# Kernel optimization log

Hardware: AMD Instinct MI355X
Metric: run time of the kernel (lower is better)

Reference implementation:

```python
import jax, jax.numpy as jnp
import numpy as np

B, T, C, H, W, NC = 128, 32, 512, 8, 32, 6625
HH = C // 2  # per-direction LSTM hidden


def setup_inputs() -> dict:
    key = jax.random.key(0)
    ks = jax.random.split(key, 20)
    u = lambda k, shape, n: jax.random.uniform(k, shape, jnp.float32, -1.0 / np.sqrt(n), 1.0 / np.sqrt(n))
    return dict(
        feature=jax.random.normal(ks[0], (B, C, H, W), jnp.float32),
        attention_map=jax.random.uniform(ks[1], (B, T, H, W), jnp.float32) + 1e-3,
        text=jax.random.randint(ks[2], (B, T), 0, NC),
        text_length=jnp.full((B,), T, dtype=jnp.int32),
        char_embeddings=jax.random.normal(ks[3], (NC, C), jnp.float32),
        lstm_w_ih_f=u(ks[4], (4 * HH, C), HH),
        lstm_w_hh_f=u(ks[5], (4 * HH, HH), HH),
        lstm_b_ih_f=u(ks[6], (4 * HH,), HH),
        lstm_b_hh_f=u(ks[7], (4 * HH,), HH),
        lstm_w_ih_b=u(ks[8], (4 * HH, C), HH),
        lstm_w_hh_b=u(ks[9], (4 * HH, HH), HH),
        lstm_b_ih_b=u(ks[10], (4 * HH,), HH),
        lstm_b_hh_b=u(ks[11], (4 * HH,), HH),
        gru_w_ih=u(ks[12], (3 * C, 2 * C), C),
        gru_w_hh=u(ks[13], (3 * C, C), C),
        gru_b_ih=u(ks[14], (3 * C,), C),
        gru_b_hh=u(ks[15], (3 * C,), C),
        gen_w=u(ks[16], (NC, C), C),
        gen_b=u(ks[17], (NC,), C),
    )


def _lstm_dir(xs, w_ih, w_hh, b_ih, b_hh):
    # xs: [T, B, C] -> hs: [T, B, HH]; PyTorch gate order i, f, g, o
    b = xs.shape[1]
    hh = w_hh.shape[1]
    def step(carry, xt):
        h, c = carry
        g = xt @ w_ih.T + h @ w_hh.T + (b_ih + b_hh)
        i, f, gg, o = jnp.split(g, 4, axis=-1)
        c = jax.nn.sigmoid(f) * c + jax.nn.sigmoid(i) * jnp.tanh(gg)
        h = jax.nn.sigmoid(o) * jnp.tanh(c)
        return (h, c), h
    h0 = jnp.zeros((b, hh), xs.dtype)
    _, hs = jax.lax.scan(step, (h0, h0), xs)
    return hs


def reference(feature, attention_map, text, text_length, char_embeddings,
              lstm_w_ih_f, lstm_w_hh_f, lstm_b_ih_f, lstm_b_hh_f,
              lstm_w_ih_b, lstm_w_hh_b, lstm_b_ih_b, lstm_b_hh_b,
              gru_w_ih, gru_w_hh, gru_b_ih, gru_b_hh, gen_w, gen_b):
    b, c, h, w = feature.shape
    t = attention_map.shape[1]
    # normalize attention over spatial dims, attention-pool features: [T, B, C]
    att = attention_map / attention_map.sum(axis=(2, 3), keepdims=True)
    cseq = jnp.einsum('bchw,bthw->tbc', feature, att)
    # bidirectional LSTM (dropout is identity in eval mode)
    hs_f = _lstm_dir(cseq, lstm_w_ih_f, lstm_w_hh_f, lstm_b_ih_f, lstm_b_hh_f)
    hs_b = _lstm_dir(cseq[::-1], lstm_w_ih_b, lstm_w_hh_b, lstm_b_ih_b, lstm_b_hh_b)[::-1]
    cseq = jnp.concatenate([hs_f, hs_b], axis=-1)  # [T, B, C]
    # teacher-forced previous-char embeddings: step 0 uses index 0
    prev_idx = jnp.concatenate([jnp.zeros((b, 1), text.dtype), text[:, :-1]], axis=1)  # [B, T]
    prev_emb = jnp.transpose(char_embeddings[prev_idx], (1, 0, 2))  # [T, B, C]
    # GRUCell decode; PyTorch gate order r, z, n
    def gru_step(hid, inp):
        ct, pe = inp
        x = jnp.concatenate([ct, pe], axis=-1)  # [B, 2C]
        gi = x @ gru_w_ih.T + gru_b_ih
        gh = hid @ gru_w_hh.T + gru_b_hh
        ir, iz, inn = jnp.split(gi, 3, axis=-1)
        hr, hz, hn = jnp.split(gh, 3, axis=-1)
        r = jax.nn.sigmoid(ir + hr)
        z = jax.nn.sigmoid(iz + hz)
        n = jnp.tanh(inn + r * hn)
        hid = (1.0 - z) * n + z * hid
        return hid, hid
    h0 = jnp.zeros((b, c), cseq.dtype)
    _, gru_res = jax.lax.scan(gru_step, h0, (cseq, prev_emb))  # [T, B, C]
    logits = gru_res @ gen_w.T + gen_b  # [T, B, NC]
    # pack per text_length; lengths are all == T so this equals a reshape
    out_res = jnp.transpose(logits, (1, 0, 2)).reshape(b * t, -1)
    out_attentions = att.reshape(b * t, h, w)
    return (out_res, out_attentions)
```

## Files before the change

kernel.cpp:

```cpp
#include <hip/hip_runtime.h>
#include <math.h>

typedef __attribute__((ext_vector_type(8))) short sh8;
typedef __attribute__((ext_vector_type(4))) short sh4;
typedef __attribute__((ext_vector_type(4))) float f4;
typedef __attribute__((ext_vector_type(4))) unsigned u4;

__device__ inline short f2bf(float f) {
    union { float f; unsigned u; } v; v.f = f;
    unsigned u = v.u;
    return (short)((u + 0x7fffu + ((u >> 16) & 1u)) >> 16);
}
__device__ inline float sigm(float x) { return 1.f / (1.f + expf(-x)); }
__device__ inline sh8 as_sh8(u4 v) { union { u4 u; sh8 s; } c; c.u = v; return c.s; }

__device__ inline sh8 frag8(const float* __restrict__ p) {
    f4 a = *(const f4*)p;
    f4 b = *(const f4*)(p + 4);
    sh8 r;
    r[0]=f2bf(a[0]); r[1]=f2bf(a[1]); r[2]=f2bf(a[2]); r[3]=f2bf(a[3]);
    r[4]=f2bf(b[0]); r[5]=f2bf(b[1]); r[6]=f2bf(b[2]); r[7]=f2bf(b[3]);
    return r;
}

__device__ inline u4 cload_u4(const void* p) {
    u4 r;
    asm volatile("global_load_dwordx4 %0, %1, off sc0 sc1" : "=v"(r) : "v"(p));
    return r;
}
__device__ inline float ld_f32(const float* p) {
    float r;
    asm volatile("global_load_dword %0, %1, off" : "=v"(r) : "v"(p));
    return r;
}

__device__ inline void grp_signal(int* myflag, int epoch) {
    asm volatile("s_waitcnt vmcnt(0)" ::: "memory");
    __builtin_amdgcn_sched_barrier(0);
    __syncthreads();
    if (threadIdx.x == 0)
        __hip_atomic_store(myflag, epoch, __ATOMIC_RELAXED, __HIP_MEMORY_SCOPE_AGENT);
}
__device__ inline void grp_wait(const int* fbase, int nb, int epoch) {
    if (threadIdx.x < 64) {
        int lane = threadIdx.x;
        bool need = lane < nb;
        const int* fp = fbase + lane * 16;
        while (true) {
            int v = need ? __hip_atomic_load(fp, __ATOMIC_RELAXED, __HIP_MEMORY_SCOPE_AGENT)
                         : 0x7fffffff;
            if (__ballot(need && (v < epoch)) == 0ull) break;
            __builtin_amdgcn_s_sleep(1);
        }
    }
    __syncthreads();
}

__global__ void zero_ctr(int* c, int n) {
    int i = blockIdx.x * blockDim.x + threadIdx.x;
    if (i < n) c[i] = 0;
}

struct CvtPack { const float* s[7]; short* d[7]; int n4[7]; };
__global__ void cvt_bf16(CvtPack p) {
    int job = blockIdx.y;
    const f4* s = (const f4*)p.s[job];
    sh4* d = (sh4*)p.d[job];
    int n4 = p.n4[job];
    for (int i = blockIdx.x * blockDim.x + threadIdx.x; i < n4; i += gridDim.x * blockDim.x) {
        f4 v = s[i];
        sh4 o; o[0]=f2bf(v[0]); o[1]=f2bf(v[1]); o[2]=f2bf(v[2]); o[3]=f2bf(v[3]);
        d[i] = o;
    }
}

__global__ void bias_prep(const float* bihf, const float* bhhf,
                          const float* bihb, const float* bhhb, float* biasL) {
    int n = blockIdx.x * blockDim.x + threadIdx.x;
    biasL[n] = (n < 1024) ? bihf[n] + bhhf[n] : bihb[n - 1024] + bhhb[n - 1024];
}

__global__ void att_norm(const float* __restrict__ att, float* __restrict__ outA) {
    int row = blockIdx.x;
    int tid = threadIdx.x;
    const float* p = att + (size_t)row * 256;
    f4 v = *(const f4*)(p + tid * 4);
    float sum = v[0] + v[1] + v[2] + v[3];
    #pragma unroll
    for (int off = 32; off; off >>= 1) sum += __shfl_down(sum, off);
    float inv = 1.f / __shfl(sum, 0);
    f4 o; o[0]=v[0]*inv; o[1]=v[1]*inv; o[2]=v[2]*inv; o[3]=v[3]*inv;
    *(f4*)(outA + (size_t)row * 256 + tid * 4) = o;
}

__global__ __launch_bounds__(256)
void pool_gemm(const float* __restrict__ feature, const float* __restrict__ att,
               short* __restrict__ cseqb) {
    int bz = blockIdx.y;
    const float* A  = feature + (size_t)bz * 512 * 256;
    const float* Wt = att + (size_t)bz * 32 * 256;
    int wave = threadIdx.x >> 6, lane = threadIdx.x & 63, r = lane & 15, hh = lane >> 4;
    int m0 = blockIdx.x * 64 + wave * 16;
    f4 acc[2] = {};
    const float* ar = A  + (size_t)(m0 + r) * 256 + hh * 8;
    const float* w0 = Wt + (size_t)r * 256 + hh * 8;
    const float* w1 = Wt + (size_t)(16 + r) * 256 + hh * 8;
    for (int kk = 0; kk < 256; kk += 32) {
        sh8 af = frag8(ar + kk);
        acc[0] = __builtin_amdgcn_mfma_f32_16x16x32_bf16(af, frag8(w0 + kk), acc[0], 0, 0, 0);
        acc[1] = __builtin_amdgcn_mfma_f32_16x16x32_bf16(af, frag8(w1 + kk), acc[1], 0, 0, 0);
    }
    #pragma unroll
    for (int j = 0; j < 2; j++) {
        int t = j * 16 + r;
        #pragma unroll
        for (int reg = 0; reg < 4; reg++) {
            int c = m0 + hh * 4 + reg;
            cseqb[(size_t)t * 65536 + (size_t)bz * 512 + c] = f2bf(acc[j][reg]);
        }
    }
}

template<int MODE>
__global__ __launch_bounds__(256)
void gemm128(const short* __restrict__ A, const short* __restrict__ W,
             const float* __restrict__ bias1, const float* __restrict__ bias2,
             float* __restrict__ out, int M, int N, int K) {
    __shared__ short lds[2][2][4096];
    const int tid = threadIdx.x, wave = tid >> 6, lane = tid & 63;
    const int r = lane & 15, hh = lane >> 4;
    const int wm = wave >> 1, wn = wave & 1;
    const int m0 = blockIdx.x * 128, n0 = blockIdx.y * 128;

    const int c0 = tid, c1 = 256 + tid;
    const int r0 = c0 >> 2, r1 = c1 >> 2;
    const int s0 = ((c0 & 3) ^ ((r0 >> 1) & 3));
    const int s1 = ((c1 & 3) ^ ((r1 >> 1) & 3));
    const short* gA0 = A + (size_t)(m0 + r0) * K + s0 * 8;
    const short* gA1 = A + (size_t)(m0 + r1) * K + s1 * 8;
    int wr0 = n0 + r0; if (wr0 > N - 1) wr0 = N - 1;
    int wr1 = n0 + r1; if (wr1 > N - 1) wr1 = N - 1;
    const short* gW0 = W + (size_t)wr0 * K + s0 * 8;
    const short* gW1 = W + (size_t)wr1 * K + s1 * 8;
    const int lo0 = (wave * 64) * 8, lo1 = (256 + wave * 64) * 8;

    auto stage = [&](int buf, int kt) {
        int ko = kt * 32;
        __builtin_amdgcn_global_load_lds((const __attribute__((address_space(1))) void*)(gA0 + ko),
            (__attribute__((address_space(3))) void*)&lds[buf][0][lo0], 16, 0, 0);
        __builtin_amdgcn_global_load_lds((const __attribute__((address_space(1))) void*)(gA1 + ko),
            (__attribute__((address_space(3))) void*)&lds[buf][0][lo1], 16, 0, 0);
        __builtin_amdgcn_global_load_lds((const __attribute__((address_space(1))) void*)(gW0 + ko),
            (__attribute__((address_space(3))) void*)&lds[buf][1][lo0], 16, 0, 0);
        __builtin_amdgcn_global_load_lds((const __attribute__((address_space(1))) void*)(gW1 + ko),
            (__attribute__((address_space(3))) void*)&lds[buf][1][lo1], 16, 0, 0);
    };

    f4 acc[4][4] = {};
    const int NT = K / 32;
    int cur = 0;

    stage(0, 0);
    __syncthreads();
    for (int kt = 0; kt < NT; ++kt) {
        if (kt + 1 < NT) stage(cur ^ 1, kt + 1);
        const char* As = (const char*)&lds[cur][0][0];
        const char* Ws = (const char*)&lds[cur][1][0];
        sh8 a[4], b[4];
        #pragma unroll
        for (int i = 0; i < 4; i++) {
            int row = wm * 64 + i * 16 + r;
            a[i] = *(const sh8*)(As + row * 64 + ((hh ^ ((row >> 1) & 3)) * 16));
        }
        #pragma unroll
        for (int i = 0; i < 4; i++) {
            int row = wn * 64 + i * 16 + r;
            b[i] = *(const sh8*)(Ws + row * 64 + ((hh ^ ((row >> 1) & 3)) * 16));
        }
        #pragma unroll
        for (int i = 0; i < 4; i++)
            #pragma unroll
            for (int j = 0; j < 4; j++)
                acc[i][j] = __builtin_amdgcn_mfma_f32_16x16x32_bf16(a[i], b[j], acc[i][j], 0, 0, 0);
        __syncthreads();
        cur ^= 1;
    }

    float bsj[4];
    #pragma unroll
    for (int j = 0; j < 4; j++) {
        int n = n0 + wn * 64 + j * 16 + r;
        int nc = n < N ? n : N - 1;
        bsj[j] = (bias1 ? bias1[nc] : 0.f) + (bias2 ? bias2[nc] : 0.f);
    }

    float* fl = (float*)&lds[0][0][0];
    #pragma unroll
    for (int hhalf = 0; hhalf < 2; hhalf++) {
        __syncthreads();
        if (wm == hhalf) {
            #pragma unroll
            for (int i = 0; i < 4; i++)
                #pragma unroll
                for (int j = 0; j < 4; j++) {
                    int col = wn * 64 + j * 16 + r;
                    #pragma unroll
                    for (int reg = 0; reg < 4; reg++)
                        fl[(i * 16 + hh * 4 + reg) * 128 + col] = acc[i][j][reg] + bsj[j];
                }
        }
        __syncthreads();
        #pragma unroll
        for (int it = 0; it < 8; it++) {
            int c = it * 256 + tid;
            int row = c >> 5, cf4 = c & 31;
            int n = n0 + cf4 * 4;
            int mrow = m0 + hhalf * 64 + row;
            size_t orow = (MODE == 0) ? (size_t)mrow
                                      : ((size_t)(mrow & 127) * 32 + (mrow >> 7));
            if (n + 3 < N) {
                *(f4*)&out[orow * N + n] = *(const f4*)&fl[row * 128 + cf4 * 4];
            } else {
                #pragma unroll
                for (int d = 0; d < 4; d++)
                    if (n + d < N) out[orow * N + n + d] = fl[row * 128 + cf4 * 4 + d];
            }
        }
    }
}

__global__ void emb_fill(const int* __restrict__ text, const float* __restrict__ emb,
                         short* __restrict__ xcatb) {
    int n = blockIdx.x;
    int t = n >> 7, b = n & 127;
    int idx = (t == 0) ? 0 : text[b * 32 + (t - 1)];
    const f4* src = (const f4*)(emb + (size_t)idx * 512);
    sh4* dst = (sh4*)(xcatb + (size_t)n * 1024 + 512);
    for (int j = threadIdx.x; j < 128; j += 64) {
        f4 v = src[j];
        sh4 o; o[0]=f2bf(v[0]); o[1]=f2bf(v[1]); o[2]=f2bf(v[2]); o[3]=f2bf(v[3]);
        dst[j] = o;
    }
}

__global__ __launch_bounds__(128)
void lstm_chain(const float* __restrict__ xfb,
                const short* __restrict__ whhf_b, const short* __restrict__ whhb_b,
                short* __restrict__ xcatb,
                int* __restrict__ flags) {
    __shared__ short wlds[64 * 256];
    const int blk = blockIdx.x;
    const int dir = blk >> 6;
    const int mg  = (blk >> 4) & 3;
    const int ug  = blk & 15;
    const int m0 = mg * 32, u0 = ug * 16;
    const short* whh = dir ? whhb_b : whhf_b;
    const int dcol = dir ? 256 : 0;

    int* grp_flags = flags + (dir * 4 + mg) * 16 * 16;
    int* my_flag   = grp_flags + ug * 16;

    const int tid = threadIdx.x, mt = tid >> 6, lane = tid & 63;
    const int r = lane & 15, hh = lane >> 4;
    unsigned* xcat32 = (unsigned*)xcatb;

    for (int i = 0; i < 16; i++) {
        int c = i * 128 + tid;
        int col = c >> 5, off = c & 31;
        int g = col >> 4, ul = col & 15;
        sh8 v = *(const sh8*)(whh + ((size_t)(g * 256 + u0 + ul)) * 256 + off * 8);
        *(sh8*)((char*)wlds + col * 512 + ((off * 16) ^ ((col & 7) << 4))) = v;
    }
    __syncthreads();

    const int arow_m = m0 + mt * 16 + r;
    const int u = u0 + r;
    const int mb = m0 + mt * 16 + hh * 4;
    float c_state[4] = {0.f, 0.f, 0.f, 0.f};

    float xv[4][4];
    {
        const int t0 = dir ? 31 : 0;
        #pragma unroll
        for (int g = 0; g < 4; g++)
            #pragma unroll
            for (int reg = 0; reg < 4; reg++)
                xv[g][reg] = xfb[((size_t)t0 * 128 + mb + reg) * 2048 + dir * 1024 + g * 256 + u];
    }

    for (int s = 0; s < 32; s++) {
        const int t = dir ? (31 - s) : s;
        f4 acc[4] = {};
        if (s > 0) {
            grp_wait(grp_flags, 16, s);
            const int tp = dir ? (t + 1) : (t - 1);
            const short* arow = xcatb + ((size_t)tp * 128 + arow_m) * 1024 + dcol + hh * 8;
            u4 afr[8];
            #pragma unroll
            for (int kk = 0; kk < 8; kk++) afr[kk] = cload_u4(arow + kk * 32);
            asm volatile("s_waitcnt vmcnt(0)" ::: "memory");
            __builtin_amdgcn_sched_barrier(0);
            #pragma unroll
            for (int kk = 0; kk < 8; kk++) {
                sh8 af = as_sh8(afr[kk]);
                #pragma unroll
                for (int g = 0; g < 4; g++) {
                    int colr = g * 16 + r;
                    sh8 bf = *(const sh8*)((const char*)wlds + colr * 512 +
                              (((kk * 64 + hh * 16)) ^ ((colr & 7) << 4)));
                    acc[g] = __builtin_amdgcn_mfma_f32_16x16x32_bf16(af, bf, acc[g], 0, 0, 0);
                }
            }
        }
        float xvn[4][4];
        if (s < 31) {
            const int tn = dir ? (t - 1) : (t + 1);
            #pragma unroll
            for (int g = 0; g < 4; g++)
                #pragma unroll
                for (int reg = 0; reg < 4; reg++)
                    xvn[g][reg] = ld_f32(&xfb[((size_t)tn * 128 + mb + reg) * 2048 + dir * 1024 + g * 256 + u]);
            asm volatile("" ::: "memory");
        }
        #pragma unroll
        for (int reg = 0; reg < 4; reg++) {
            int m = mb + reg;
            float gI = acc[0][reg] + xv[0][reg];
            float gF = acc[1][reg] + xv[1][reg];
            float gG = acc[2][reg] + xv[2][reg];
            float gO = acc[3][reg] + xv[3][reg];
            float cn = sigm(gF) * c_state[reg] + sigm(gI) * tanhf(gG);
            c_state[reg] = cn;
            float h = sigm(gO) * tanhf(cn);
            unsigned hb = (unsigned)(unsigned short)f2bf(h);
            unsigned pb = (unsigned)__shfl_xor((int)hb, 1, 64);
            if (!(r & 1))
                __hip_atomic_store(&xcat32[((size_t)t * 128 + m) * 512 + ((dcol + u) >> 1)],
                                   hb | (pb << 16), __ATOMIC_RELAXED, __HIP_MEMORY_SCOPE_AGENT);
        }
        if (s < 31) {
            grp_signal(my_flag, s + 1);
            #pragma unroll
            for (int g = 0; g < 4; g++)
                #pragma unroll
                for (int reg = 0; reg < 4; reg++)
                    xv[g][reg] = xvn[g][reg];
        }
    }
}

__global__ __launch_bounds__(128)
void gru_chain(const float* __restrict__ gi,
               const short* __restrict__ gwhh_b, const float* __restrict__ bhh,
               short* __restrict__ gresb,
               int* __restrict__ flags) {
    __shared__ short wlds[48 * 512];
    const int blk = blockIdx.x;
    const int mg = blk >> 5, ug = blk & 31;
    const int m0 = mg * 32, u0 = ug * 16;

    int* grp_flags = flags + mg * 32 * 16;
    int* my_flag   = grp_flags + ug * 16;

    const int tid = threadIdx.x, mt = tid >> 6, lane = tid & 63;
    const int r = lane & 15, hh = lane >> 4;
    unsigned* gres32 = (unsigned*)gresb;

    for (int i = 0; i < 24; i++) {
        int c = i * 128 + tid;
        int col = c >> 6, off = c & 63;
        int g = col >> 4, ul = col & 15;
        sh8 v = *(const sh8*)(gwhh_b + ((size_t)(g * 512 + u0 + ul)) * 512 + off * 8);
        *(sh8*)((char*)wlds + col * 1024 + ((off * 16) ^ ((col & 7) << 4))) = v;
    }
    __syncthreads();

    const int arow_m = m0 + mt * 16 + r;
    const int u = u0 + r;
    const int mb = m0 + mt * 16 + hh * 4;
    const float bh_r = bhh[u], bh_z = bhh[512 + u], bh_n = bhh[1024 + u];
    float h_state[4] = {0.f, 0.f, 0.f, 0.f};

    float gv[3][4];
    #pragma unroll
    for (int g = 0; g < 3; g++)
        #pragma unroll
        for (int reg = 0; reg < 4; reg++)
            gv[g][reg] = gi[((size_t)(mb + reg)) * 1536 + g * 512 + u];

    for (int t = 0; t < 32; t++) {
        f4 acc[3] = {};
        if (t > 0) {
            grp_wait(grp_flags, 32, t);
            const short* arow = gresb + ((size_t)(t - 1) * 128 + arow_m) * 512 + hh * 8;
            u4 afr[16];
            #pragma unroll
            for (int kk = 0; kk < 16; kk++) afr[kk] = cload_u4(arow + kk * 32);
            asm volatile("s_waitcnt vmcnt(0)" ::: "memory");
            __builtin_amdgcn_sched_barrier(0);
            #pragma unroll
            for (int kk = 0; kk < 16; kk++) {
                sh8 af = as_sh8(afr[kk]);
                #pragma unroll
                for (int g = 0; g < 3; g++) {
                    int colr = g * 16 + r;
                    sh8 bf = *(const sh8*)((const char*)wlds + colr * 1024 +
                              (((kk * 64 + hh * 16)) ^ ((colr & 7) << 4)));
                    acc[g] = __builtin_amdgcn_mfma_f32_16x16x32_bf16(af, bf, acc[g], 0, 0, 0);
                }
            }
        }
        float gvn[3][4];
        if (t < 31) {
            #pragma unroll
            for (int g = 0; g < 3; g++)
                #pragma unroll
                for (int reg = 0; reg < 4; reg++)
                    gvn[g][reg] = ld_f32(&gi[((size_t)(t + 1) * 128 + mb + reg) * 1536 + g * 512 + u]);
            asm volatile("" ::: "memory");
        }
        #pragma unroll
        for (int reg = 0; reg < 4; reg++) {
            int m = mb + reg;
            float rr = sigm(gv[0][reg] + acc[0][reg] + bh_r);
            float zz = sigm(gv[1][reg] + acc[1][reg] + bh_z);
            float nn = tanhf(gv[2][reg] + rr * (acc[2][reg] + bh_n));
            float h = (1.f - zz) * nn + zz * h_state[reg];
            h_state[reg] = h;
            unsigned hb = (unsigned)(unsigned short)f2bf(h);
            unsigned pb = (unsigned)__shfl_xor((int)hb, 1, 64);
            if (!(r & 1))
                __hip_atomic_store(&gres32[((size_t)t * 128 + m) * 256 + (u >> 1)],
                                   hb | (pb << 16), __ATOMIC_RELAXED, __HIP_MEMORY_SCOPE_AGENT);
        }
        if (t < 31) {
            grp_signal(my_flag, t + 1);
            #pragma unroll
            for (int g = 0; g < 3; g++)
                #pragma unroll
                for (int reg = 0; reg < 4; reg++)
                    gv[g][reg] = gvn[g][reg];
        }
    }
}

extern "C" void kernel_launch(void* const* d_in, const int* in_sizes, int n_in,
                              void* d_out, int out_size, void* d_ws, size_t ws_size,
                              hipStream_t stream) {
    const float* feature = (const float*)d_in[0];
    const float* attmap  = (const float*)d_in[1];
    const int*   text    = (const int*)d_in[2];
    const float* cemb    = (const float*)d_in[4];
    const float* wihf    = (const float*)d_in[5];
    const float* whhf    = (const float*)d_in[6];
    const float* bihf    = (const float*)d_in[7];
    const float* bhhf    = (const float*)d_in[8];
    const float* wihb    = (const float*)d_in[9];
    const float* whhb    = (const float*)d_in[10];
    const float* bihb    = (const float*)d_in[11];
    const float* bhhb    = (const float*)d_in[12];
    const float* gwih    = (const float*)d_in[13];
    const float* gwhh    = (const float*)d_in[14];
    const float* gbih    = (const float*)d_in[15];
    const float* gbhh    = (const float*)d_in[16];
    const float* genw    = (const float*)d_in[17];
    const float* genb    = (const float*)d_in[18];

    float* out    = (float*)d_out;
    float* outAtt = out + (size_t)4096 * 6625;

    float* xfb   = (float*)d_ws;
    float* gi    = xfb + 8388608;
    float* biasL = gi + 6291456;
    int*   flags = (int*)(biasL + 2048);
    short* cseqb  = (short*)(flags + 4096);
    short* xcatb  = cseqb + 2097152;
    short* gresb  = xcatb + 4194304;
    short* wih_b  = gresb + 2097152;
    short* whhf_b = wih_b + 1048576;
    short* whhb_b = whhf_b + 262144;
    short* gwih_b = whhb_b + 262144;
    short* gwhh_b = gwih_b + 1572864;
    short* genw_b = gwhh_b + 786432;

    zero_ctr<<<dim3(16), dim3(256), 0, stream>>>(flags, 4096);

    CvtPack p;
    p.s[0] = wihf; p.d[0] = wih_b;           p.n4[0] = 524288 / 4;
    p.s[1] = wihb; p.d[1] = wih_b + 524288;  p.n4[1] = 524288 / 4;
    p.s[2] = whhf; p.d[2] = whhf_b;          p.n4[2] = 262144 / 4;
    p.s[3] = whhb; p.d[3] = whhb_b;          p.n4[3] = 262144 / 4;
    p.s[4] = gwih; p.d[4] = gwih_b;          p.n4[4] = 1572864 / 4;
    p.s[5] = gwhh; p.d[5] = gwhh_b;          p.n4[5] = 786432 / 4;
    p.s[6] = genw; p.d[6] = genw_b;          p.n4[6] = 3392000 / 4;
    cvt_bf16<<<dim3(128, 7), dim3(256), 0, stream>>>(p);
    bias_prep<<<dim3(8), dim3(256), 0, stream>>>(bihf, bhhf, bihb, bhhb, biasL);

    att_norm<<<dim3(4096), dim3(64), 0, stream>>>(attmap, outAtt);
    pool_gemm<<<dim3(8, 128), dim3(256), 0, stream>>>(feature, outAtt, cseqb);

    gemm128<0><<<dim3(32, 16), dim3(256), 0, stream>>>(cseqb, wih_b, biasL, nullptr,
                                                       xfb, 4096, 2048, 512);
    emb_fill<<<dim3(4096), dim3(64), 0, stream>>>(text, cemb, xcatb);

    lstm_chain<<<dim3(128), dim3(128), 0, stream>>>(xfb, whhf_b, whhb_b, xcatb, flags);

    gemm128<0><<<dim3(32, 12), dim3(256), 0, stream>>>(xcatb, gwih_b, gbih, nullptr,
                                                       gi, 4096, 1536, 1024);

    gru_chain<<<dim3(128), dim3(128), 0, stream>>>(gi, gwhh_b, gbhh, gresb, flags + 2048);

    gemm128<1><<<dim3(32, 52), dim3(256), 0, stream>>>(gresb, genw_b, genb, nullptr,
                                                       out, 4096, 6625, 512);
}
```

Before: 439.0 us.

## Repartition LSTM/GRU recurrent chains into fewer, wider blocks with smaller sync groups

Re-tiles the recurrent LSTM kernel from 128 blocks (32 rows x 16 units) to 64 blocks (16 rows x 64 units, with all four gates held in 128KB of dynamic LDS). The GRU kernel goes to 16-row x 32-unit tiles using 96KB of LDS. Each step's flag barrier now waits on 4 and 16 peers instead of 16 and 32, which cuts cross-block synchronisation cost on the serial critical path. It also swaps expf/tanhf for fast exp2/rcp intrinsics and moves the next-step input loads after the signal. Risks are fewer active CUs, less precise activations, and exposed load latency for the next-step inputs.

```diff
diff --git a/kernel.cpp b/kernel.cpp
--- a/kernel.cpp
+++ b/kernel.cpp
@@ -11,8 +11,10 @@
     unsigned u = v.u;
     return (short)((u + 0x7fffu + ((u >> 16) & 1u)) >> 16);
 }
-__device__ inline float sigm(float x) { return 1.f / (1.f + expf(-x)); }
 __device__ inline sh8 as_sh8(u4 v) { union { u4 u; sh8 s; } c; c.u = v; return c.s; }
+
+__device__ inline float sigm(float x)  { return __builtin_amdgcn_rcpf(1.f + __builtin_amdgcn_exp2f(-1.44269504f * x)); }
+__device__ inline float tanha(float x) { return 1.f - 2.f * __builtin_amdgcn_rcpf(1.f + __builtin_amdgcn_exp2f(2.88539008f * x)); }
 
 __device__ inline sh8 frag8(const float* __restrict__ p) {
     f4 a = *(const f4*)p;
@@ -26,11 +28,6 @@
 __device__ inline u4 cload_u4(const void* p) {
     u4 r;
     asm volatile("global_load_dwordx4 %0, %1, off sc0 sc1" : "=v"(r) : "v"(p));
-    return r;
-}
-__device__ inline float ld_f32(const float* p) {
-    float r;
-    asm volatile("global_load_dword %0, %1, off" : "=v"(r) : "v"(p));
     return r;
 }
 
@@ -248,53 +245,54 @@
                 const short* __restrict__ whhf_b, const short* __restrict__ whhb_b,
                 short* __restrict__ xcatb,
                 int* __restrict__ flags) {
-    __shared__ short wlds[64 * 256];
+    extern __shared__ short wlds[];
     const int blk = blockIdx.x;
-    const int dir = blk >> 6;
-    const int mg  = (blk >> 4) & 3;
-    const int ug  = blk & 15;
-    const int m0 = mg * 32, u0 = ug * 16;
+    const int dir = blk >> 5;
+    const int mg  = (blk >> 2) & 7;
+    const int ug  = blk & 3;
+    const int m0 = mg * 16, u0 = ug * 64;
     const short* whh = dir ? whhb_b : whhf_b;
     const int dcol = dir ? 256 : 0;
 
-    int* grp_flags = flags + (dir * 4 + mg) * 16 * 16;
+    int* grp_flags = flags + (dir * 8 + mg) * 4 * 16;
     int* my_flag   = grp_flags + ug * 16;
 
-    const int tid = threadIdx.x, mt = tid >> 6, lane = tid & 63;
+    const int tid = threadIdx.x, w = tid >> 6, lane = tid & 63;
     const int r = lane & 15, hh = lane >> 4;
     unsigned* xcat32 = (unsigned*)xcatb;
 
-    for (int i = 0; i < 16; i++) {
+    for (int i = 0; i < 64; i++) {
         int c = i * 128 + tid;
         int col = c >> 5, off = c & 31;
-        int g = col >> 4, ul = col & 15;
+        int g = col >> 6, ul = col & 63;
         sh8 v = *(const sh8*)(whh + ((size_t)(g * 256 + u0 + ul)) * 256 + off * 8);
         *(sh8*)((char*)wlds + col * 512 + ((off * 16) ^ ((col & 7) << 4))) = v;
     }
     __syncthreads();
 
-    const int arow_m = m0 + mt * 16 + r;
-    const int u = u0 + r;
-    const int mb = m0 + mt * 16 + hh * 4;
-    float c_state[4] = {0.f, 0.f, 0.f, 0.f};
-
-    float xv[4][4];
+    const int mb = m0 + hh * 4;
+    float c_state[2][4] = {};
+
+    float xv[4][2][4];
     {
         const int t0 = dir ? 31 : 0;
         #pragma unroll
         for (int g = 0; g < 4; g++)
             #pragma unroll
-            for (int reg = 0; reg < 4; reg++)
-                xv[g][reg] = xfb[((size_t)t0 * 128 + mb + reg) * 2048 + dir * 1024 + g * 256 + u];
+            for (int j = 0; j < 2; j++)
+                #pragma unroll
+                for (int reg = 0; reg < 4; reg++)
+                    xv[g][j][reg] = xfb[((size_t)t0 * 128 + mb + reg) * 2048 + dir * 1024
+                                        + g * 256 + u0 + w * 32 + j * 16 + r];
     }
 
     for (int s = 0; s < 32; s++) {
         const int t = dir ? (31 - s) : s;
-        f4 acc[4] = {};
+        f4 acc[4][2] = {};
         if (s > 0) {
-            grp_wait(grp_flags, 16, s);
+            grp_wait(grp_flags, 4, s);
             const int tp = dir ? (t + 1) : (t - 1);
-            const short* arow = xcatb + ((size_t)tp * 128 + arow_m) * 1024 + dcol + hh * 8;
+            const short* arow = xcatb + ((size_t)tp * 128 + m0 + r) * 1024 + dcol + hh * 8;
             u4 afr[8];
             #pragma unroll
             for (int kk = 0; kk < 8; kk++) afr[kk] = cload_u4(arow + kk * 32);
@@ -304,47 +302,46 @@
             for (int kk = 0; kk < 8; kk++) {
                 sh8 af = as_sh8(afr[kk]);
                 #pragma unroll
-                for (int g = 0; g < 4; g++) {
-                    int colr = g * 16 + r;
-                    sh8 bf = *(const sh8*)((const char*)wlds + colr * 512 +
-                              (((kk * 64 + hh * 16)) ^ ((colr & 7) << 4)));
-                    acc[g] = __builtin_amdgcn_mfma_f32_16x16x32_bf16(af, bf, acc[g], 0, 0, 0);
-                }
+                for (int g = 0; g < 4; g++)
+                    #pragma unroll
+                    for (int j = 0; j < 2; j++) {
+                        int colr = g * 64 + w * 32 + j * 16 + r;
+                        sh8 bf = *(const sh8*)((const char*)wlds + colr * 512 +
+                                  ((kk * 64 + hh * 16) ^ ((colr & 7) << 4)));
+                        acc[g][j] = __builtin_amdgcn_mfma_f32_16x16x32_bf16(af, bf, acc[g][j], 0, 0, 0);
+                    }
             }
         }
-        float xvn[4][4];
-        if (s < 31) {
-            const int tn = dir ? (t - 1) : (t + 1);
-            #pragma unroll
-            for (int g = 0; g < 4; g++)
-                #pragma unroll
-                for (int reg = 0; reg < 4; reg++)
-                    xvn[g][reg] = ld_f32(&xfb[((size_t)tn * 128 + mb + reg) * 2048 + dir * 1024 + g * 256 + u]);
-            asm volatile("" ::: "memory");
-        }
-        #pragma unroll
-        for (int reg = 0; reg < 4; reg++) {
-            int m = mb + reg;
-            float gI = acc[0][reg] + xv[0][reg];
-            float gF = acc[1][reg] + xv[1][reg];
-            float gG = acc[2][reg] + xv[2][reg];
-            float gO = acc[3][reg] + xv[3][reg];
-            float cn = sigm(gF) * c_state[reg] + sigm(gI) * tanhf(gG);
-            c_state[reg] = cn;
-            float h = sigm(gO) * tanhf(cn);
-            unsigned hb = (unsigned)(unsigned short)f2bf(h);
-            unsigned pb = (unsigned)__shfl_xor((int)hb, 1, 64);
-            if (!(r & 1))
-                __hip_atomic_store(&xcat32[((size_t)t * 128 + m) * 512 + ((dcol + u) >> 1)],
-                                   hb | (pb << 16), __ATOMIC_RELAXED, __HIP_MEMORY_SCOPE_AGENT);
-        }
+        #pragma unroll
+        for (int j = 0; j < 2; j++)
+            #pragma unroll
+            for (int reg = 0; reg < 4; reg++) {
+                int m = mb + reg;
+                int u = u0 + w * 32 + j * 16 + r;
+                float gI = acc[0][j][reg] + xv[0][j][reg];
+                float gF = acc[1][j][reg] + xv[1][j][reg];
+                float gG = acc[2][j][reg] + xv[2][j][reg];
+                float gO = acc[3][j][reg] + xv[3][j][reg];
+                float cn = sigm(gF) * c_state[j][reg] + sigm(gI) * tanha(gG);
+                c_state[j][reg] = cn;
+                float h = sigm(gO) * tanha(cn);
+                unsigned hb = (unsigned)(unsigned short)f2bf(h);
+                unsigned pb = (unsigned)__shfl_xor((int)hb, 1, 64);
+                if (!(r & 1))
+                    __hip_atomic_store(&xcat32[((size_t)t * 128 + m) * 512 + ((dcol + u) >> 1)],
+                                       hb | (pb << 16), __ATOMIC_RELAXED, __HIP_MEMORY_SCOPE_AGENT);
+            }
         if (s < 31) {
             grp_signal(my_flag, s + 1);
+            const int tn = dir ? (t - 1) : (t + 1);
             #pragma unroll
             for (int g = 0; g < 4; g++)
                 #pragma unroll
-                for (int reg = 0; reg < 4; reg++)
-                    xv[g][reg] = xvn[g][reg];
+                for (int j = 0; j < 2; j++)
+                    #pragma unroll
+                    for (int reg = 0; reg < 4; reg++)
+                        xv[g][j][reg] = xfb[((size_t)tn * 128 + mb + reg) * 2048 + dir * 1024
+                                            + g * 256 + u0 + w * 32 + j * 16 + r];
         }
     }
 }
@@ -354,30 +351,29 @@
                const short* __restrict__ gwhh_b, const float* __restrict__ bhh,
                short* __restrict__ gresb,
                int* __restrict__ flags) {
-    __shared__ short wlds[48 * 512];
+    extern __shared__ short wlds[];
     const int blk = blockIdx.x;
-    const int mg = blk >> 5, ug = blk & 31;
-    const int m0 = mg * 32, u0 = ug * 16;
-
-    int* grp_flags = flags + mg * 32 * 16;
+    const int mg = blk >> 4, ug = blk & 15;
+    const int m0 = mg * 16, u0 = ug * 32;
+
+    int* grp_flags = flags + mg * 16 * 16;
     int* my_flag   = grp_flags + ug * 16;
 
-    const int tid = threadIdx.x, mt = tid >> 6, lane = tid & 63;
+    const int tid = threadIdx.x, w = tid >> 6, lane = tid & 63;
     const int r = lane & 15, hh = lane >> 4;
     unsigned* gres32 = (unsigned*)gresb;
 
-    for (int i = 0; i < 24; i++) {
+    for (int i = 0; i < 48; i++) {
         int c = i * 128 + tid;
         int col = c >> 6, off = c & 63;
-        int g = col >> 4, ul = col & 15;
+        int g = col >> 5, ul = col & 31;
         sh8 v = *(const sh8*)(gwhh_b + ((size_t)(g * 512 + u0 + ul)) * 512 + off * 8);
         *(sh8*)((char*)wlds + col * 1024 + ((off * 16) ^ ((col & 7) << 4))) = v;
     }
     __syncthreads();
 
-    const int arow_m = m0 + mt * 16 + r;
-    const int u = u0 + r;
-    const int mb = m0 + mt * 16 + hh * 4;
+    const int mb = m0 + hh * 4;
+    const int u = u0 + w * 16 + r;
     const float bh_r = bhh[u], bh_z = bhh[512 + u], bh_n = bhh[1024 + u];
     float h_state[4] = {0.f, 0.f, 0.f, 0.f};
 
@@ -391,8 +387,8 @@
     for (int t = 0; t < 32; t++) {
         f4 acc[3] = {};
         if (t > 0) {
-            grp_wait(grp_flags, 32, t);
-            const short* arow = gresb + ((size_t)(t - 1) * 128 + arow_m) * 512 + hh * 8;
+            grp_wait(grp_flags, 16, t);
+            const short* arow = gresb + ((size_t)(t - 1) * 128 + m0 + r) * 512 + hh * 8;
             u4 afr[16];
             #pragma unroll
             for (int kk = 0; kk < 16; kk++) afr[kk] = cload_u4(arow + kk * 32);
@@ -403,28 +399,19 @@
                 sh8 af = as_sh8(afr[kk]);
                 #pragma unroll
                 for (int g = 0; g < 3; g++) {
-                    int colr = g * 16 + r;
+                    int colr = g * 32 + w * 16 + r;
                     sh8 bf = *(const sh8*)((const char*)wlds + colr * 1024 +
-                              (((kk * 64 + hh * 16)) ^ ((colr & 7) << 4)));
+                              ((kk * 64 + hh * 16) ^ ((colr & 7) << 4)));
                     acc[g] = __builtin_amdgcn_mfma_f32_16x16x32_bf16(af, bf, acc[g], 0, 0, 0);
                 }
             }
-        }
-        float gvn[3][4];
-        if (t < 31) {
-            #pragma unroll
-            for (int g = 0; g < 3; g++)
-                #pragma unroll
-                for (int reg = 0; reg < 4; reg++)
-                    gvn[g][reg] = ld_f32(&gi[((size_t)(t + 1) * 128 + mb + reg) * 1536 + g * 512 + u]);
-            asm volatile("" ::: "memory");
         }
         #pragma unroll
         for (int reg = 0; reg < 4; reg++) {
             int m = mb + reg;
             float rr = sigm(gv[0][reg] + acc[0][reg] + bh_r);
             float zz = sigm(gv[1][reg] + acc[1][reg] + bh_z);
-            float nn = tanhf(gv[2][reg] + rr * (acc[2][reg] + bh_n));
+            float nn = tanha(gv[2][reg] + rr * (acc[2][reg] + bh_n));
             float h = (1.f - zz) * nn + zz * h_state[reg];
             h_state[reg] = h;
             unsigned hb = (unsigned)(unsigned short)f2bf(h);
@@ -439,7 +426,7 @@
             for (int g = 0; g < 3; g++)
                 #pragma unroll
                 for (int reg = 0; reg < 4; reg++)
-                    gv[g][reg] = gvn[g][reg];
+                    gv[g][reg] = gi[((size_t)(t + 1) * 128 + mb + reg) * 1536 + g * 512 + u];
         }
     }
 }
@@ -483,6 +470,11 @@
     short* gwhh_b = gwih_b + 1572864;
     short* genw_b = gwhh_b + 786432;
 
+    hipFuncSetAttribute((const void*)lstm_chain,
+                        hipFuncAttributeMaxDynamicSharedMemorySize, 131072);
+    hipFuncSetAttribute((const void*)gru_chain,
+                        hipFuncAttributeMaxDynamicSharedMemorySize, 98304);
+
     zero_ctr<<<dim3(16), dim3(256), 0, stream>>>(flags, 4096);
 
     CvtPack p;
@@ -503,12 +495,12 @@
                                                        xfb, 4096, 2048, 512);
     emb_fill<<<dim3(4096), dim3(64), 0, stream>>>(text, cemb, xcatb);
 
-    lstm_chain<<<dim3(128), dim3(128), 0, stream>>>(xfb, whhf_b, whhb_b, xcatb, flags);
+    lstm_chain<<<dim3(64), dim3(128), 131072, stream>>>(xfb, whhf_b, whhb_b, xcatb, flags);
 
     gemm128<0><<<dim3(32, 12), dim3(256), 0, stream>>>(xcatb, gwih_b, gbih, nullptr,
                                                        gi, 4096, 1536, 1024);
 
-    gru_chain<<<dim3(128), dim3(128), 0, stream>>>(gi, gwhh_b, gbhh, gresb, flags + 2048);
+    gru_chain<<<dim3(128), dim3(128), 98304, stream>>>(gi, gwhh_b, gbhh, gresb, flags + 1024);
 
     gemm128<1><<<dim3(32, 52), dim3(256), 0, stream>>>(gresb, genw_b, genb, nullptr,
                                                        out, 4096, 6625, 512);
```

Measured after the change: 420.0 us. -4.3%, faster.

## Regroup GRU chain into 16-row groups, use fast exp/rcp activations

Applied to the files above, without the earlier changes.

The GRU recurrence is repartitioned so each block handles 16 batch rows and 32 hidden units, which halves the number of peers in each flag-wait group from 32 to 16. Each block now holds a 96 KB slice of the recurrent weight in dynamic shared memory. Sigmoid and tanh in both the LSTM and GRU chains use hardware exp2/rcp intrinsics instead of expf/tanhf, cutting latency on the serial critical path at some accuracy cost. The explicit prefetch of next-step input gates is replaced by a plain load issued after the signal.

```diff
diff --git a/kernel.cpp b/kernel.cpp
--- a/kernel.cpp
+++ b/kernel.cpp
@@ -11,8 +11,10 @@
     unsigned u = v.u;
     return (short)((u + 0x7fffu + ((u >> 16) & 1u)) >> 16);
 }
-__device__ inline float sigm(float x) { return 1.f / (1.f + expf(-x)); }
 __device__ inline sh8 as_sh8(u4 v) { union { u4 u; sh8 s; } c; c.u = v; return c.s; }
+
+__device__ inline float sigm(float x)  { return __builtin_amdgcn_rcpf(1.f + __builtin_amdgcn_exp2f(-1.44269504f * x)); }
+__device__ inline float tanha(float x) { return 1.f - 2.f * __builtin_amdgcn_rcpf(1.f + __builtin_amdgcn_exp2f(2.88539008f * x)); }
 
 __device__ inline sh8 frag8(const float* __restrict__ p) {
     f4 a = *(const f4*)p;
@@ -26,11 +28,6 @@
 __device__ inline u4 cload_u4(const void* p) {
     u4 r;
     asm volatile("global_load_dwordx4 %0, %1, off sc0 sc1" : "=v"(r) : "v"(p));
-    return r;
-}
-__device__ inline float ld_f32(const float* p) {
-    float r;
-    asm volatile("global_load_dword %0, %1, off" : "=v"(r) : "v"(p));
     return r;
 }
 
@@ -312,16 +309,6 @@
                 }
             }
         }
-        float xvn[4][4];
-        if (s < 31) {
-            const int tn = dir ? (t - 1) : (t + 1);
-            #pragma unroll
-            for (int g = 0; g < 4; g++)
-                #pragma unroll
-                for (int reg = 0; reg < 4; reg++)
-                    xvn[g][reg] = ld_f32(&xfb[((size_t)tn * 128 + mb + reg) * 2048 + dir * 1024 + g * 256 + u]);
-            asm volatile("" ::: "memory");
-        }
         #pragma unroll
         for (int reg = 0; reg < 4; reg++) {
             int m = mb + reg;
@@ -329,9 +316,9 @@
             float gF = acc[1][reg] + xv[1][reg];
             float gG = acc[2][reg] + xv[2][reg];
             float gO = acc[3][reg] + xv[3][reg];
-            float cn = sigm(gF) * c_state[reg] + sigm(gI) * tanhf(gG);
+            float cn = sigm(gF) * c_state[reg] + sigm(gI) * tanha(gG);
             c_state[reg] = cn;
-            float h = sigm(gO) * tanhf(cn);
+            float h = sigm(gO) * tanha(cn);
             unsigned hb = (unsigned)(unsigned short)f2bf(h);
             unsigned pb = (unsigned)__shfl_xor((int)hb, 1, 64);
             if (!(r & 1))
@@ -340,11 +327,12 @@
         }
         if (s < 31) {
             grp_signal(my_flag, s + 1);
+            const int tn = dir ? (t - 1) : (t + 1);
             #pragma unroll
             for (int g = 0; g < 4; g++)
                 #pragma unroll
                 for (int reg = 0; reg < 4; reg++)
-                    xv[g][reg] = xvn[g][reg];
+                    xv[g][reg] = xfb[((size_t)tn * 128 + mb + reg) * 2048 + dir * 1024 + g * 256 + u];
         }
     }
 }
@@ -354,30 +342,29 @@
                const short* __restrict__ gwhh_b, const float* __restrict__ bhh,
                short* __restrict__ gresb,
                int* __restrict__ flags) {
-    __shared__ short wlds[48 * 512];
+    extern __shared__ short wlds[];
     const int blk = blockIdx.x;
-    const int mg = blk >> 5, ug = blk & 31;
-    const int m0 = mg * 32, u0 = ug * 16;
-
-    int* grp_flags = flags + mg * 32 * 16;
+    const int mg = blk >> 4, ug = blk & 15;
+    const int m0 = mg * 16, u0 = ug * 32;
+
+    int* grp_flags = flags + mg * 16 * 16;
     int* my_flag   = grp_flags + ug * 16;
 
-    const int tid = threadIdx.x, mt = tid >> 6, lane = tid & 63;
+    const int tid = threadIdx.x, w = tid >> 6, lane = tid & 63;
     const int r = lane & 15, hh = lane >> 4;
     unsigned* gres32 = (unsigned*)gresb;
 
-    for (int i = 0; i < 24; i++) {
+    for (int i = 0; i < 48; i++) {
         int c = i * 128 + tid;
         int col = c >> 6, off = c & 63;
-        int g = col >> 4, ul = col & 15;
+        int g = col >> 5, ul = col & 31;
         sh8 v = *(const sh8*)(gwhh_b + ((size_t)(g * 512 + u0 + ul)) * 512 + off * 8);
         *(sh8*)((char*)wlds + col * 1024 + ((off * 16) ^ ((col & 7) << 4))) = v;
     }
     __syncthreads();
 
-    const int arow_m = m0 + mt * 16 + r;
-    const int u = u0 + r;
-    const int mb = m0 + mt * 16 + hh * 4;
+    const int mb = m0 + hh * 4;
+    const int u = u0 + w * 16 + r;
     const float bh_r = bhh[u], bh_z = bhh[512 + u], bh_n = bhh[1024 + u];
     float h_state[4] = {0.f, 0.f, 0.f, 0.f};
 
@@ -391,8 +378,8 @@
     for (int t = 0; t < 32; t++) {
         f4 acc[3] = {};
         if (t > 0) {
-            grp_wait(grp_flags, 32, t);
-            const short* arow = gresb + ((size_t)(t - 1) * 128 + arow_m) * 512 + hh * 8;
+            grp_wait(grp_flags, 16, t);
+            const short* arow = gresb + ((size_t)(t - 1) * 128 + m0 + r) * 512 + hh * 8;
             u4 afr[16];
             #pragma unroll
             for (int kk = 0; kk < 16; kk++) afr[kk] = cload_u4(arow + kk * 32);
@@ -403,28 +390,19 @@
                 sh8 af = as_sh8(afr[kk]);
                 #pragma unroll
                 for (int g = 0; g < 3; g++) {
-                    int colr = g * 16 + r;
+                    int colr = g * 32 + w * 16 + r;
                     sh8 bf = *(const sh8*)((const char*)wlds + colr * 1024 +
-                              (((kk * 64 + hh * 16)) ^ ((colr & 7) << 4)));
+                              ((kk * 64 + hh * 16) ^ ((colr & 7) << 4)));
                     acc[g] = __builtin_amdgcn_mfma_f32_16x16x32_bf16(af, bf, acc[g], 0, 0, 0);
                 }
             }
-        }
-        float gvn[3][4];
-        if (t < 31) {
-            #pragma unroll
-            for (int g = 0; g < 3; g++)
-                #pragma unroll
-                for (int reg = 0; reg < 4; reg++)
-                    gvn[g][reg] = ld_f32(&gi[((size_t)(t + 1) * 128 + mb + reg) * 1536 + g * 512 + u]);
-            asm volatile("" ::: "memory");
         }
         #pragma unroll
         for (int reg = 0; reg < 4; reg++) {
             int m = mb + reg;
             float rr = sigm(gv[0][reg] + acc[0][reg] + bh_r);
             float zz = sigm(gv[1][reg] + acc[1][reg] + bh_z);
-            float nn = tanhf(gv[2][reg] + rr * (acc[2][reg] + bh_n));
+            float nn = tanha(gv[2][reg] + rr * (acc[2][reg] + bh_n));
             float h = (1.f - zz) * nn + zz * h_state[reg];
             h_state[reg] = h;
             unsigned hb = (unsigned)(unsigned short)f2bf(h);
@@ -439,7 +417,7 @@
             for (int g = 0; g < 3; g++)
                 #pragma unroll
                 for (int reg = 0; reg < 4; reg++)
-                    gv[g][reg] = gvn[g][reg];
+                    gv[g][reg] = gi[((size_t)(t + 1) * 128 + mb + reg) * 1536 + g * 512 + u];
         }
     }
 }
@@ -483,6 +461,9 @@
     short* gwhh_b = gwih_b + 1572864;
     short* genw_b = gwhh_b + 786432;
 
+    hipFuncSetAttribute((const void*)gru_chain,
+                        hipFuncAttributeMaxDynamicSharedMemorySize, 98304);
+
     zero_ctr<<<dim3(16), dim3(256), 0, stream>>>(flags, 4096);
 
     CvtPack p;
@@ -508,7 +489,7 @@
     gemm128<0><<<dim3(32, 12), dim3(256), 0, stream>>>(xcatb, gwih_b, gbih, nullptr,
                                                        gi, 4096, 1536, 1024);
 
-    gru_chain<<<dim3(128), dim3(128), 0, stream>>>(gi, gwhh_b, gbhh, gresb, flags + 2048);
+    gru_chain<<<dim3(128), dim3(128), 98304, stream>>>(gi, gwhh_b, gbhh, gresb, flags + 2048);
 
     gemm128<1><<<dim3(32, 52), dim3(256), 0, stream>>>(gresb, genw_b, genb, nullptr,
                                                        out, 4096, 6625, 512);
```

Measured after the change: 385.7 us. 12.2% less time.
